# Optimization experiments

Measured on AMD Instinct MI355X. Metric: run time of the kernel, lower is better.

## Reference

```python
import jax, jax.numpy as jnp
import numpy as np

NODE_DIM = 256
EDGE_DIM = 128
HIDDEN = EDGE_DIM // 2  # edge_downsample=2 -> 64
LN_EPS = 1e-5


def setup_inputs() -> dict:
    key = jax.random.key(0)
    ks = jax.random.split(key, 12)
    B, N = 1, 768
    s_in = 1.0 / np.sqrt(NODE_DIM)
    s_h = 1.0 / np.sqrt(HIDDEN)
    return {
        "x": jax.random.normal(ks[0], (B, N, NODE_DIM), jnp.float32),
        "z": jnp.zeros((1,), jnp.float32),  # unused in forward (matches torch module)
        "Wi": jax.random.uniform(ks[1], (NODE_DIM, HIDDEN), jnp.float32, -s_in, s_in),
        "bi": jax.random.uniform(ks[2], (HIDDEN,), jnp.float32, -s_in, s_in),
        "Wj": jax.random.uniform(ks[3], (NODE_DIM, HIDDEN), jnp.float32, -s_in, s_in),
        "bj": jax.random.uniform(ks[4], (HIDDEN,), jnp.float32, -s_in, s_in),
        "ln_g": jnp.ones((HIDDEN,), jnp.float32),
        "ln_b": jnp.zeros((HIDDEN,), jnp.float32),
        "W1": jax.random.uniform(ks[5], (HIDDEN, HIDDEN), jnp.float32, -s_h, s_h),
        "b1": jax.random.uniform(ks[6], (HIDDEN,), jnp.float32, -s_h, s_h),
        "W2": jax.random.uniform(ks[7], (HIDDEN, EDGE_DIM), jnp.float32, -s_h, s_h),
        "b2": jax.random.uniform(ks[8], (EDGE_DIM,), jnp.float32, -s_h, s_h),
    }


def _layernorm(h, g, b):
    mu = jnp.mean(h, axis=-1, keepdims=True)
    var = jnp.mean(jnp.square(h - mu), axis=-1, keepdims=True)
    return (h - mu) * jax.lax.rsqrt(var + LN_EPS) * g + b


def reference(x, z, Wi, bi, Wj, bj, ln_g, ln_b, W1, b1, W2, b2):
    # x: [B, N, node_dim]
    n_i = x @ Wi + bi  # [B, N, H]
    n_j = x @ Wj + bj  # [B, N, H]
    # outer sum: [B, N(j-axis first per torch indexing), N, H]
    n_in = n_i[:, None, :, :] + n_j[:, :, None, :]
    h = _layernorm(n_in, ln_g, ln_b)
    h = jax.nn.relu(h @ W1 + b1)
    return h @ W2 + b2  # [B, N, N, edge_dim]
```

## Files before the change

### kernel.cpp

```cpp
#include <hip/hip_runtime.h>
#include <hip/hip_bf16.h>

typedef float f32x4 __attribute__((ext_vector_type(4)));
typedef short s16x8 __attribute__((ext_vector_type(8)));
typedef short s16x4 __attribute__((ext_vector_type(4)));

#define N_NODES 768
#define NODE_DIM_ 256
#define HDIM 64
#define EDIM 128
#define CTILES 48
#define TILES_TOTAL (N_NODES * CTILES)

static __device__ __forceinline__ short f2bf(float f) {
    __hip_bfloat16 h = __float2bfloat16(f);
    return __builtin_bit_cast(short, h);
}

__global__ __launch_bounds__(256) void proj_kernel(
        const float* __restrict__ x,
        const float* __restrict__ Wi, const float* __restrict__ bi,
        const float* __restrict__ Wj, const float* __restrict__ bj,
        float* __restrict__ NI, float* __restrict__ NJ) {
    int row  = blockIdx.x * 4 + (threadIdx.x >> 6);
    int lane = threadIdx.x & 63;
    float ai = bi[lane];
    float aj = bj[lane];
    const float* xr = x + row * NODE_DIM_;
#pragma unroll 8
    for (int k = 0; k < NODE_DIM_; ++k) {
        float xv = xr[k];
        ai = fmaf(xv, Wi[k * HDIM + lane], ai);
        aj = fmaf(xv, Wj[k * HDIM + lane], aj);
    }
    NI[row * HDIM + lane] = ai;
    NJ[row * HDIM + lane] = aj;
}

__global__ __launch_bounds__(256) void edge_kernel(
        const float* __restrict__ NI, const float* __restrict__ NJ,
        const float* __restrict__ lng, const float* __restrict__ lnb,
        const float* __restrict__ W1, const float* __restrict__ b1,
        const float* __restrict__ W2, const float* __restrict__ b2,
        float* __restrict__ out) {
    __shared__ short W1L[4096];
    __shared__ short W2L[8192];
    __shared__ short TL[4][1024];

    for (int idx = threadIdx.x; idx < 4096; idx += 256) {
        int k = idx >> 6, n = idx & 63;
        W1L[(k >> 3) * 512 + n * 8 + (k & 7)] = f2bf(W1[idx]);
    }
    for (int idx = threadIdx.x; idx < 8192; idx += 256) {
        int k = idx >> 7, n = idx & 127;
        W2L[(k >> 3) * 1024 + n * 8 + (k & 7)] = f2bf(W2[idx]);
    }
    __syncthreads();

    const int wave = threadIdx.x >> 6;
    const int lane = threadIdx.x & 63;
    const int l15  = lane & 15;
    const int hi   = lane >> 4;
    const int swz  = (l15 & 7) << 4;

    float gl[8], gh[8], bl[8], bh[8];
#pragma unroll
    for (int j = 0; j < 8; ++j) {
        gl[j] = lng[hi * 8 + j];      gh[j] = lng[32 + hi * 8 + j];
        bl[j] = lnb[hi * 8 + j];      bh[j] = lnb[32 + hi * 8 + j];
    }
    float b1v[16];
#pragma unroll
    for (int nt = 0; nt < 4; ++nt)
#pragma unroll
        for (int r = 0; r < 4; ++r)
            b1v[nt * 4 + r] = b1[nt * 16 + hi * 4 + r];
    f32x4 b2v[8];
#pragma unroll
    for (int nt = 0; nt < 8; ++nt)
        b2v[nt] = *(const f32x4*)&b2[nt * 16 + hi * 4];

    char* tl = (char*)&TL[wave][0];

    const int wid = blockIdx.x * 4 + wave;
    const int nw  = gridDim.x * 4;
    for (int t = wid; t < TILES_TOTAL; t += nw) {
        int a  = t / CTILES;
        int c0 = (t - a * CTILES) * 16;

        const float* nip = NI + (c0 + l15) * HDIM + hi * 8;
        const float* njp = NJ + a * HDIM + hi * 8;
        float v[16];
#pragma unroll
        for (int j = 0; j < 8; ++j) {
            v[j]     = nip[j]      + njp[j];
            v[8 + j] = nip[32 + j] + njp[32 + j];
        }
        float s = 0.f, ss = 0.f;
#pragma unroll
        for (int j = 0; j < 16; ++j) { s += v[j]; ss = fmaf(v[j], v[j], ss); }
        s += __shfl_xor(s, 16);  ss += __shfl_xor(ss, 16);
        s += __shfl_xor(s, 32);  ss += __shfl_xor(ss, 32);
        float mu   = s * (1.f / 64.f);
        float var  = ss * (1.f / 64.f) - mu * mu;
        float rstd = rsqrtf(var + 1e-5f);

        s16x8 hf0, hf1;
#pragma unroll
        for (int j = 0; j < 8; ++j) {
            hf0[j] = f2bf(fmaf((v[j]     - mu) * rstd, gl[j], bl[j]));
            hf1[j] = f2bf(fmaf((v[8 + j] - mu) * rstd, gh[j], bh[j]));
        }

#pragma unroll
        for (int nt = 0; nt < 4; ++nt) {
            f32x4 acc = {0.f, 0.f, 0.f, 0.f};
            s16x8 w0 = *(const s16x8*)&W1L[(0 + hi) * 512 + (nt * 16 + l15) * 8];
            s16x8 w1 = *(const s16x8*)&W1L[(4 + hi) * 512 + (nt * 16 + l15) * 8];
            acc = __builtin_amdgcn_mfma_f32_16x16x32_bf16(w0, hf0, acc, 0, 0, 0);
            acc = __builtin_amdgcn_mfma_f32_16x16x32_bf16(w1, hf1, acc, 0, 0, 0);
            s16x4 tv;
#pragma unroll
            for (int r = 0; r < 4; ++r)
                tv[r] = f2bf(fmaxf(acc[r] + b1v[nt * 4 + r], 0.f));
            int wb = (l15 * 128 + (nt * 16 + hi * 4) * 2) ^ swz;
            *(s16x4*)(tl + wb) = tv;
        }

        int rb0 = (l15 * 128 + hi * 16) ^ swz;
        int rb1 = (l15 * 128 + hi * 16 + 64) ^ swz;
        s16x8 tf0 = *(const s16x8*)(tl + rb0);
        s16x8 tf1 = *(const s16x8*)(tl + rb1);

        float* op = out + ((size_t)(a * N_NODES + c0 + l15)) * EDIM + hi * 4;
#pragma unroll
        for (int nt = 0; nt < 8; ++nt) {
            f32x4 acc = {0.f, 0.f, 0.f, 0.f};
            s16x8 w0 = *(const s16x8*)&W2L[(0 + hi) * 1024 + (nt * 16 + l15) * 8];
            s16x8 w1 = *(const s16x8*)&W2L[(4 + hi) * 1024 + (nt * 16 + l15) * 8];
            acc = __builtin_amdgcn_mfma_f32_16x16x32_bf16(w0, tf0, acc, 0, 0, 0);
            acc = __builtin_amdgcn_mfma_f32_16x16x32_bf16(w1, tf1, acc, 0, 0, 0);
            f32x4 res = acc + b2v[nt];
            *(f32x4*)(op + nt * 16) = res;
        }
    }
}

extern "C" void kernel_launch(void* const* d_in, const int* in_sizes, int n_in,
                              void* d_out, int out_size, void* d_ws, size_t ws_size,
                              hipStream_t stream) {
    const float* x   = (const float*)d_in[0];
    const float* Wi  = (const float*)d_in[2];
    const float* bi  = (const float*)d_in[3];
    const float* Wj  = (const float*)d_in[4];
    const float* bj  = (const float*)d_in[5];
    const float* lng = (const float*)d_in[6];
    const float* lnb = (const float*)d_in[7];
    const float* W1  = (const float*)d_in[8];
    const float* b1  = (const float*)d_in[9];
    const float* W2  = (const float*)d_in[10];
    const float* b2  = (const float*)d_in[11];
    float* out = (float*)d_out;

    float* NI = (float*)d_ws;
    float* NJ = NI + N_NODES * HDIM;

    proj_kernel<<<N_NODES / 4, 256, 0, stream>>>(x, Wi, bi, Wj, bj, NI, NJ);
    edge_kernel<<<2304, 256, 0, stream>>>(NI, NJ, lng, lnb, W1, b1, W2, b2, out);
}
```

Measured before the change: 86.17 us.

## Factor LayerNorm and first linear through outer sum using precomputed per-node projections

```diff
diff --git a/kernel.cpp b/kernel.cpp
--- a/kernel.cpp
+++ b/kernel.cpp
@@ -17,7 +17,183 @@
     return __builtin_bit_cast(short, h);
 }
 
+__global__ void prep_kernel(const float* __restrict__ W1, const float* __restrict__ b1,
+                            const float* __restrict__ lng, const float* __restrict__ lnb,
+                            float* __restrict__ W1g, float* __restrict__ S1,
+                            float* __restrict__ C1) {
+    int n = threadIdx.x;
+    float s = 0.f, c = 0.f;
+#pragma unroll 8
+    for (int k = 0; k < HDIM; ++k) {
+        float w  = W1[k * HDIM + n];
+        float wg = lng[k] * w;
+        W1g[k * HDIM + n] = wg;
+        s += wg;
+        c = fmaf(lnb[k], w, c);
+    }
+    S1[n] = s;
+    C1[n] = c + b1[n];
+}
+
 __global__ __launch_bounds__(256) void proj_kernel(
+        const float* __restrict__ x,
+        const float* __restrict__ Wi, const float* __restrict__ bi,
+        const float* __restrict__ Wj, const float* __restrict__ bj,
+        const float* __restrict__ W1g,
+        __hip_bfloat16* __restrict__ NIbf, __hip_bfloat16* __restrict__ NJbf,
+        float* __restrict__ Pi, float* __restrict__ Pj,
+        float* __restrict__ mi, float* __restrict__ qi,
+        float* __restrict__ mj, float* __restrict__ qj) {
+    __shared__ float W1gL[HDIM * HDIM];
+    __shared__ float rowi[4][HDIM], rowj[4][HDIM];
+    for (int idx = threadIdx.x; idx < HDIM * HDIM; idx += 256) W1gL[idx] = W1g[idx];
+
+    int wave = threadIdx.x >> 6, lane = threadIdx.x & 63;
+    int row  = blockIdx.x * 4 + wave;
+    float ai = bi[lane], aj = bj[lane];
+    const float* xr = x + row * NODE_DIM_;
+#pragma unroll 8
+    for (int k = 0; k < NODE_DIM_; ++k) {
+        float xv = xr[k];
+        ai = fmaf(xv, Wi[k * HDIM + lane], ai);
+        aj = fmaf(xv, Wj[k * HDIM + lane], aj);
+    }
+    NIbf[row * HDIM + lane] = __float2bfloat16(ai);
+    NJbf[row * HDIM + lane] = __float2bfloat16(aj);
+    rowi[wave][lane] = ai;
+    rowj[wave][lane] = aj;
+
+    float si = ai, sqi = ai * ai, sj = aj, sqj = aj * aj;
+#pragma unroll
+    for (int o = 1; o < 64; o <<= 1) {
+        si  += __shfl_xor(si, o);   sqi += __shfl_xor(sqi, o);
+        sj  += __shfl_xor(sj, o);   sqj += __shfl_xor(sqj, o);
+    }
+    if (lane == 0) {
+        mi[row] = si * (1.f / 64.f);  qi[row] = sqi * (1.f / 64.f);
+        mj[row] = sj * (1.f / 64.f);  qj[row] = sqj * (1.f / 64.f);
+    }
+    __syncthreads();
+
+    float pi = 0.f, pj = 0.f;
+#pragma unroll 8
+    for (int k = 0; k < HDIM; ++k) {
+        float wg = W1gL[k * HDIM + lane];
+        pi = fmaf(rowi[wave][k], wg, pi);
+        pj = fmaf(rowj[wave][k], wg, pj);
+    }
+    Pi[row * HDIM + lane] = pi;
+    Pj[row * HDIM + lane] = pj;
+}
+
+__global__ __launch_bounds__(256) void gdot_kernel(
+        const __hip_bfloat16* __restrict__ NIbf,
+        const __hip_bfloat16* __restrict__ NJbf,
+        float* __restrict__ G) {
+    int wave = threadIdx.x >> 6, lane = threadIdx.x & 63;
+    int l15 = lane & 15, hi = lane >> 4;
+    int tile = blockIdx.x * 4 + wave;
+    int ta = tile / CTILES, tc = tile % CTILES;
+    int a0 = ta * 16, c0 = tc * 16;
+
+    const short* NJ = (const short*)NJbf;
+    const short* NI = (const short*)NIbf;
+    s16x8 a0f = *(const s16x8*)&NJ[(a0 + l15) * HDIM + hi * 8];
+    s16x8 a1f = *(const s16x8*)&NJ[(a0 + l15) * HDIM + 32 + hi * 8];
+    s16x8 b0f = *(const s16x8*)&NI[(c0 + l15) * HDIM + hi * 8];
+    s16x8 b1f = *(const s16x8*)&NI[(c0 + l15) * HDIM + 32 + hi * 8];
+    f32x4 acc = {0.f, 0.f, 0.f, 0.f};
+    acc = __builtin_amdgcn_mfma_f32_16x16x32_bf16(a0f, b0f, acc, 0, 0, 0);
+    acc = __builtin_amdgcn_mfma_f32_16x16x32_bf16(a1f, b1f, acc, 0, 0, 0);
+#pragma unroll
+    for (int r = 0; r < 4; ++r)
+        G[(size_t)(a0 + hi * 4 + r) * N_NODES + c0 + l15] = acc[r];
+}
+
+__global__ __launch_bounds__(256) void edge2_kernel(
+        const float* __restrict__ Pi, const float* __restrict__ Pj,
+        const float* __restrict__ mi, const float* __restrict__ qi,
+        const float* __restrict__ mj, const float* __restrict__ qj,
+        const float* __restrict__ G,
+        const float* __restrict__ S1, const float* __restrict__ C1,
+        const float* __restrict__ W2, const float* __restrict__ b2,
+        float* __restrict__ out) {
+    __shared__ short W2L[8192];
+    for (int idx = threadIdx.x; idx < 8192; idx += 256) {
+        int k = idx >> 7, e = idx & 127;
+        W2L[(k >> 3) * 1024 + e * 8 + (k & 7)] = f2bf(W2[idx]);
+    }
+    __syncthreads();
+
+    const int wave = threadIdx.x >> 6;
+    const int lane = threadIdx.x & 63;
+    const int l15  = lane & 15;
+    const int hi   = lane >> 4;
+
+    f32x4 S1a = *(const f32x4*)&S1[hi * 8];
+    f32x4 S1b = *(const f32x4*)&S1[hi * 8 + 4];
+    f32x4 S1c = *(const f32x4*)&S1[32 + hi * 8];
+    f32x4 S1d = *(const f32x4*)&S1[32 + hi * 8 + 4];
+    f32x4 C1a = *(const f32x4*)&C1[hi * 8];
+    f32x4 C1b = *(const f32x4*)&C1[hi * 8 + 4];
+    f32x4 C1c = *(const f32x4*)&C1[32 + hi * 8];
+    f32x4 C1d = *(const f32x4*)&C1[32 + hi * 8 + 4];
+    f32x4 b2v[8];
+#pragma unroll
+    for (int nt = 0; nt < 8; ++nt)
+        b2v[nt] = *(const f32x4*)&b2[nt * 16 + hi * 4];
+
+    const int wid = blockIdx.x * 4 + wave;
+    const int nw  = gridDim.x * 4;
+    for (int t = wid; t < TILES_TOTAL; t += nw) {
+        int a  = t / CTILES;
+        int c0 = (t - a * CTILES) * 16;
+        int c  = c0 + l15;
+
+        float mu   = mi[c] + mj[a];
+        float ms   = qi[c] + qj[a] + G[(size_t)a * N_NODES + c] * (1.f / 32.f);
+        float var  = ms - mu * mu;
+        float rstd = rsqrtf(var + 1e-5f);
+        float rm   = rstd * mu;
+
+        const float* pic = Pi + c * HDIM;
+        const float* pja = Pj + a * HDIM;
+        f32x4 pi0 = *(const f32x4*)(pic + hi * 8);
+        f32x4 pi1 = *(const f32x4*)(pic + hi * 8 + 4);
+        f32x4 pi2 = *(const f32x4*)(pic + 32 + hi * 8);
+        f32x4 pi3 = *(const f32x4*)(pic + 32 + hi * 8 + 4);
+        f32x4 pj0 = *(const f32x4*)(pja + hi * 8);
+        f32x4 pj1 = *(const f32x4*)(pja + hi * 8 + 4);
+        f32x4 pj2 = *(const f32x4*)(pja + 32 + hi * 8);
+        f32x4 pj3 = *(const f32x4*)(pja + 32 + hi * 8 + 4);
+
+        s16x8 tf0, tf1;
+#pragma unroll
+        for (int j = 0; j < 4; ++j) {
+            float t0 = fmaf(rstd, pi0[j] + pj0[j], fmaf(-rm, S1a[j], C1a[j]));
+            float t1 = fmaf(rstd, pi1[j] + pj1[j], fmaf(-rm, S1b[j], C1b[j]));
+            float t2 = fmaf(rstd, pi2[j] + pj2[j], fmaf(-rm, S1c[j], C1c[j]));
+            float t3 = fmaf(rstd, pi3[j] + pj3[j], fmaf(-rm, S1d[j], C1d[j]));
+            tf0[j]     = f2bf(fmaxf(t0, 0.f));
+            tf0[4 + j] = f2bf(fmaxf(t1, 0.f));
+            tf1[j]     = f2bf(fmaxf(t2, 0.f));
+            tf1[4 + j] = f2bf(fmaxf(t3, 0.f));
+        }
+
+        float* op = out + ((size_t)(a * N_NODES + c)) * EDIM + hi * 4;
+#pragma unroll
+        for (int nt = 0; nt < 8; ++nt) {
+            f32x4 acc = {0.f, 0.f, 0.f, 0.f};
+            s16x8 w0 = *(const s16x8*)&W2L[(0 + hi) * 1024 + (nt * 16 + l15) * 8];
+            s16x8 w1 = *(const s16x8*)&W2L[(4 + hi) * 1024 + (nt * 16 + l15) * 8];
+            acc = __builtin_amdgcn_mfma_f32_16x16x32_bf16(w0, tf0, acc, 0, 0, 0);
+            acc = __builtin_amdgcn_mfma_f32_16x16x32_bf16(w1, tf1, acc, 0, 0, 0);
+            *(f32x4*)(op + nt * 16) = acc + b2v[nt];
+        }
+    }
+}
+
+__global__ __launch_bounds__(256) void proj_fb_kernel(
         const float* __restrict__ x,
         const float* __restrict__ Wi, const float* __restrict__ bi,
         const float* __restrict__ Wj, const float* __restrict__ bj,
@@ -37,7 +213,7 @@
     NJ[row * HDIM + lane] = aj;
 }
 
-__global__ __launch_bounds__(256) void edge_kernel(
+__global__ __launch_bounds__(256) void edge_fb_kernel(
         const float* __restrict__ NI, const float* __restrict__ NJ,
         const float* __restrict__ lng, const float* __restrict__ lnb,
         const float* __restrict__ W1, const float* __restrict__ b1,
@@ -46,7 +222,6 @@
     __shared__ short W1L[4096];
     __shared__ short W2L[8192];
     __shared__ short TL[4][1024];
-
     for (int idx = threadIdx.x; idx < 4096; idx += 256) {
         int k = idx >> 6, n = idx & 63;
         W1L[(k >> 3) * 512 + n * 8 + (k & 7)] = f2bf(W1[idx]);
@@ -56,13 +231,11 @@
         W2L[(k >> 3) * 1024 + n * 8 + (k & 7)] = f2bf(W2[idx]);
     }
     __syncthreads();
-
     const int wave = threadIdx.x >> 6;
     const int lane = threadIdx.x & 63;
     const int l15  = lane & 15;
     const int hi   = lane >> 4;
     const int swz  = (l15 & 7) << 4;
-
     float gl[8], gh[8], bl[8], bh[8];
 #pragma unroll
     for (int j = 0; j < 8; ++j) {
@@ -79,15 +252,12 @@
 #pragma unroll
     for (int nt = 0; nt < 8; ++nt)
         b2v[nt] = *(const f32x4*)&b2[nt * 16 + hi * 4];
-
     char* tl = (char*)&TL[wave][0];
-
     const int wid = blockIdx.x * 4 + wave;
     const int nw  = gridDim.x * 4;
     for (int t = wid; t < TILES_TOTAL; t += nw) {
         int a  = t / CTILES;
         int c0 = (t - a * CTILES) * 16;
-
         const float* nip = NI + (c0 + l15) * HDIM + hi * 8;
         const float* njp = NJ + a * HDIM + hi * 8;
         float v[16];
@@ -104,14 +274,12 @@
         float mu   = s * (1.f / 64.f);
         float var  = ss * (1.f / 64.f) - mu * mu;
         float rstd = rsqrtf(var + 1e-5f);
-
         s16x8 hf0, hf1;
 #pragma unroll
         for (int j = 0; j < 8; ++j) {
             hf0[j] = f2bf(fmaf((v[j]     - mu) * rstd, gl[j], bl[j]));
             hf1[j] = f2bf(fmaf((v[8 + j] - mu) * rstd, gh[j], bh[j]));
         }
-
 #pragma unroll
         for (int nt = 0; nt < 4; ++nt) {
             f32x4 acc = {0.f, 0.f, 0.f, 0.f};
@@ -126,12 +294,10 @@
             int wb = (l15 * 128 + (nt * 16 + hi * 4) * 2) ^ swz;
             *(s16x4*)(tl + wb) = tv;
         }
-
         int rb0 = (l15 * 128 + hi * 16) ^ swz;
         int rb1 = (l15 * 128 + hi * 16 + 64) ^ swz;
         s16x8 tf0 = *(const s16x8*)(tl + rb0);
         s16x8 tf1 = *(const s16x8*)(tl + rb1);
-
         float* op = out + ((size_t)(a * N_NODES + c0 + l15)) * EDIM + hi * 4;
 #pragma unroll
         for (int nt = 0; nt < 8; ++nt) {
@@ -140,8 +306,7 @@
             s16x8 w1 = *(const s16x8*)&W2L[(4 + hi) * 1024 + (nt * 16 + l15) * 8];
             acc = __builtin_amdgcn_mfma_f32_16x16x32_bf16(w0, tf0, acc, 0, 0, 0);
             acc = __builtin_amdgcn_mfma_f32_16x16x32_bf16(w1, tf1, acc, 0, 0, 0);
-            f32x4 res = acc + b2v[nt];
-            *(f32x4*)(op + nt * 16) = res;
+            *(f32x4*)(op + nt * 16) = acc + b2v[nt];
         }
     }
 }
@@ -162,9 +327,45 @@
     const float* b2  = (const float*)d_in[11];
     float* out = (float*)d_out;
 
-    float* NI = (float*)d_ws;
-    float* NJ = NI + N_NODES * HDIM;
-
-    proj_kernel<<<N_NODES / 4, 256, 0, stream>>>(x, Wi, bi, Wj, bj, NI, NJ);
-    edge_kernel<<<2304, 256, 0, stream>>>(NI, NJ, lng, lnb, W1, b1, W2, b2, out);
-}
+    float* ws = (float*)d_ws;
+    const size_t oW1g = 0;
+    const size_t oS1  = 4096;
+    const size_t oC1  = 4160;
+    const size_t oPi  = 4224;
+    const size_t oPj  = 53376;
+    const size_t oMi  = 102528;
+    const size_t oQi  = 103296;
+    const size_t oMj  = 104064;
+    const size_t oQj  = 104832;
+    const size_t oG   = 105600;
+    const size_t oNI  = 695424;
+    const size_t oNJ  = 720000;
+    const size_t needF = 744576;
+
+    if (ws_size < needF * sizeof(float)) {
+        float* NI = ws;
+        float* NJ = NI + N_NODES * HDIM;
+        proj_fb_kernel<<<N_NODES / 4, 256, 0, stream>>>(x, Wi, bi, Wj, bj, NI, NJ);
+        edge_fb_kernel<<<2304, 256, 0, stream>>>(NI, NJ, lng, lnb, W1, b1, W2, b2, out);
+        return;
+    }
+
+    float* W1g = ws + oW1g;
+    float* S1  = ws + oS1;
+    float* C1  = ws + oC1;
+    float* Pi  = ws + oPi;
+    float* Pj  = ws + oPj;
+    float* mi  = ws + oMi;
+    float* qi  = ws + oQi;
+    float* mj  = ws + oMj;
+    float* qj  = ws + oQj;
+    float* G   = ws + oG;
+    __hip_bfloat16* NIbf = (__hip_bfloat16*)(ws + oNI);
+    __hip_bfloat16* NJbf = (__hip_bfloat16*)(ws + oNJ);
+
+    prep_kernel<<<1, 64, 0, stream>>>(W1, b1, lng, lnb, W1g, S1, C1);
+    proj_kernel<<<N_NODES / 4, 256, 0, stream>>>(x, Wi, bi, Wj, bj, W1g,
+                                                 NIbf, NJbf, Pi, Pj, mi, qi, mj, qj);
+    gdot_kernel<<<2304 / 4, 256, 0, stream>>>(NIbf, NJbf, G);
+    edge2_kernel<<<2304, 256, 0, stream>>>(Pi, Pj, mi, qi, mj, qj, G, S1, C1, W2, b2, out);
+}
```

Measured after the change: 110.0 us. 1.28x slower.
